# Optimization experiments

Measured on AMD Instinct MI355X. Metric: run time of the kernel, lower is better.

## Reference

```python
import jax, jax.numpy as jnp
import numpy as np
from jax import lax

B, T, F, K = 128, 1024, 128, 32


def setup_inputs() -> dict:
    key = jax.random.key(0)
    k1, k2, k3 = jax.random.split(key, 3)
    inp = jax.random.normal(k1, (B, T, F), dtype=jnp.float32)
    mask = jnp.ones((B, T), dtype=bool)
    W_emit = jax.random.normal(k2, (F, K), dtype=jnp.float32) * 0.02
    transition = jax.random.normal(k3, (K, K), dtype=jnp.float32) * 0.1
    return {"input": inp, "mask": mask, "W_emit": W_emit, "transition": transition}


def reference(input, mask, W_emit, transition):
    # emissions: [B, T, K]
    emission = jnp.einsum('btf,fk->btk', input, W_emit)
    alpha0 = emission[:, 0]                      # [B, K]
    em_seq = jnp.swapaxes(emission[:, 1:], 0, 1)  # [T-1, B, K]
    mk_seq = jnp.swapaxes(mask[:, 1:], 0, 1)      # [T-1, B]

    def step(alpha, xs):
        em_t, m_t = xs
        # alpha_t[b,j] = logsumexp_i(alpha[b,i] + transition[i,j]) + em_t[b,j]
        new = jax.scipy.special.logsumexp(alpha[:, :, None] + transition[None], axis=1) + em_t
        alpha = jnp.where(m_t[:, None], new, alpha)
        return alpha, None

    alpha, _ = lax.scan(step, alpha0, (em_seq, mk_seq))
    log_z = jax.scipy.special.logsumexp(alpha, axis=-1)  # [B]
    return jnp.sum(log_z)
```

## Files before the change

### kernel.cpp

```cpp
#include <hip/hip_runtime.h>
#include <hip/hip_bf16.h>

#define Bb 128
#define Tt 1024
#define Ff 128
#define Kk 32
#define KE 36
#define LOG32 3.4657359027997265f

typedef __attribute__((ext_vector_type(8))) short bf16x8;
typedef __attribute__((ext_vector_type(4))) float f32x4;
typedef __attribute__((ext_vector_type(16))) float f32x16;

__device__ __forceinline__ float bf2f(unsigned u) {
    return __uint_as_float(u << 16);
}
__device__ __forceinline__ unsigned bfpk2(float a, float b) {
    __hip_bfloat162 h = __float22bfloat162_rn(make_float2(a, b));
    unsigned u;
    __builtin_memcpy(&u, &h, sizeof(u));
    return u;
}
__device__ __forceinline__ void plswap(unsigned &a, unsigned &b) {
    asm("v_permlane32_swap_b32 %0, %1" : "+v"(a), "+v"(b));
}

__global__ __launch_bounds__(64, 4) void chunk_kernel(
    const float* __restrict__ inp, const int* __restrict__ mask,
    const float* __restrict__ W, const float* __restrict__ trans,
    unsigned short* __restrict__ SQ, float* __restrict__ out)
{
    __shared__ __align__(16) float gl[32 * KE];
    const int lane = threadIdx.x & 63;
    const int q = (lane >> 4) & 3, n = lane & 15;
    const int c32 = lane & 31, hi = lane >> 5;
    const int b = blockIdx.x >> 5, c = blockIdx.x & 31;
    const int t0 = c * 32;

    if (blockIdx.x == 0 && lane == 0) out[0] = 0.f;

    const int* mbp = mask + (long)b * Tt;
    unsigned mbits = (unsigned)__ballot(mbp[t0 + c32] != 0);
    if (c == 0) mbits &= ~1u;

    bf16x8 Wlo[4], Whi[4];
    #pragma unroll
    for (int kt = 0; kt < 4; ++kt) {
        const int f0 = kt * 32 + q * 8;
        float wl[8], wh[8];
        #pragma unroll
        for (int jj = 0; jj < 8; ++jj) {
            wl[jj] = W[(f0 + jj) * Kk + n];
            wh[jj] = W[(f0 + jj) * Kk + 16 + n];
        }
        uint4 uc = make_uint4(bfpk2(wl[0], wl[1]), bfpk2(wl[2], wl[3]),
                              bfpk2(wl[4], wl[5]), bfpk2(wl[6], wl[7]));
        uint4 ud = make_uint4(bfpk2(wh[0], wh[1]), bfpk2(wh[2], wh[3]),
                              bfpk2(wh[4], wh[5]), bfpk2(wh[6], wh[7]));
        Wlo[kt] = __builtin_bit_cast(bf16x8, uc);
        Whi[kt] = __builtin_bit_cast(bf16x8, ud);
    }

    const f32x4 zz = {0.f, 0.f, 0.f, 0.f};
    #pragma unroll
    for (int s = 0; s < 2; ++s) {
        f32x4 E0 = zz, E1 = zz;
        const float* xrow = inp + ((long)b * Tt + t0 + s * 16) * Ff;
        #pragma unroll
        for (int kt = 0; kt < 4; ++kt) {
            const int f0 = kt * 32 + q * 8;
            float4 a0v = *(const float4*)&xrow[n * Ff + f0];
            float4 a1v = *(const float4*)&xrow[n * Ff + f0 + 4];
            uint4 ua = make_uint4(bfpk2(a0v.x, a0v.y), bfpk2(a0v.z, a0v.w),
                                  bfpk2(a1v.x, a1v.y), bfpk2(a1v.z, a1v.w));
            bf16x8 Aw = __builtin_bit_cast(bf16x8, ua);
            E0 = __builtin_amdgcn_mfma_f32_16x16x32_bf16(Aw, Wlo[kt], E0, 0, 0, 0);
            E1 = __builtin_amdgcn_mfma_f32_16x16x32_bf16(Aw, Whi[kt], E1, 0, 0, 0);
        }
        #pragma unroll
        for (int r = 0; r < 4; ++r) {
            gl[(s * 16 + q * 4 + r) * KE + n]      = __expf(E0[r] - LOG32);
            gl[(s * 16 + q * 4 + r) * KE + 16 + n] = __expf(E1[r] - LOG32);
        }
    }

    float Elo[8], Ehi[8];
    #pragma unroll
    for (int j = 0; j < 8; ++j) {
        Elo[j] = __expf(trans[(8 * hi + j) * Kk + c32]);
        Ehi[j] = __expf(trans[(16 + 8 * hi + j) * Kk + c32]);
    }

    unsigned B1[4], B2[4];
    #pragma unroll
    for (int w2 = 0; w2 < 4; ++w2) {
        const int r0 = 8 * hi + 2 * w2;
        B1[w2] = (r0 == c32 ? 0x3f80u : 0u) | (r0 + 1 == c32 ? (0x3f80u << 16) : 0u);
        const int r2 = 16 + r0;
        B2[w2] = (r2 == c32 ? 0x3f80u : 0u) | (r2 + 1 == c32 ? (0x3f80u << 16) : 0u);
    }

    #pragma unroll
    for (int ls = 0; ls < 32; ++ls) {
        if (!((mbits >> ls) & 1u)) continue;
        const float g = gl[ls * KE + c32];
        uint4 fa = make_uint4(bfpk2(g * Elo[0], g * Elo[1]), bfpk2(g * Elo[2], g * Elo[3]),
                              bfpk2(g * Elo[4], g * Elo[5]), bfpk2(g * Elo[6], g * Elo[7]));
        uint4 fb = make_uint4(bfpk2(g * Ehi[0], g * Ehi[1]), bfpk2(g * Ehi[2], g * Ehi[3]),
                              bfpk2(g * Ehi[4], g * Ehi[5]), bfpk2(g * Ehi[6], g * Ehi[7]));
        bf16x8 Alo = __builtin_bit_cast(bf16x8, fa);
        bf16x8 Ahi = __builtin_bit_cast(bf16x8, fb);
        uint4 ub1 = make_uint4(B1[0], B1[1], B1[2], B1[3]);
        uint4 ub2 = make_uint4(B2[0], B2[1], B2[2], B2[3]);
        f32x16 Cc = {0.f, 0.f, 0.f, 0.f, 0.f, 0.f, 0.f, 0.f,
                     0.f, 0.f, 0.f, 0.f, 0.f, 0.f, 0.f, 0.f};
        Cc = __builtin_amdgcn_mfma_f32_32x32x16_bf16(Alo, __builtin_bit_cast(bf16x8, ub1), Cc, 0, 0, 0);
        Cc = __builtin_amdgcn_mfma_f32_32x32x16_bf16(Ahi, __builtin_bit_cast(bf16x8, ub2), Cc, 0, 0, 0);
        unsigned wa = bfpk2(Cc[0], Cc[1]),   wb = bfpk2(Cc[2], Cc[3]);
        unsigned xa = bfpk2(Cc[4], Cc[5]),   xb = bfpk2(Cc[6], Cc[7]);
        unsigned ya = bfpk2(Cc[8], Cc[9]),   yb = bfpk2(Cc[10], Cc[11]);
        unsigned za = bfpk2(Cc[12], Cc[13]), zb = bfpk2(Cc[14], Cc[15]);
        plswap(wa, xa); B1[0] = wa; B1[2] = xa;
        plswap(wb, xb); B1[1] = wb; B1[3] = xb;
        plswap(ya, za); B2[0] = ya; B2[2] = za;
        plswap(yb, zb); B2[1] = yb; B2[3] = zb;
    }

    unsigned short* sq = SQ + (long)(b * 32 + c) * 1024;
    #pragma unroll
    for (int w2 = 0; w2 < 4; ++w2) {
        const int r0 = 8 * hi + 2 * w2;
        sq[ r0      * 32 + c32] = (unsigned short)(B1[w2] & 0xffffu);
        sq[(r0 + 1) * 32 + c32] = (unsigned short)(B1[w2] >> 16);
        const int r2 = 16 + r0;
        sq[ r2      * 32 + c32] = (unsigned short)(B2[w2] & 0xffffu);
        sq[(r2 + 1) * 32 + c32] = (unsigned short)(B2[w2] >> 16);
    }
}

__global__ __launch_bounds__(64) void apply_kernel(
    const float* __restrict__ inp, const int* __restrict__ mask,
    const float* __restrict__ W, const unsigned short* __restrict__ SQ,
    float* __restrict__ out)
{
    const int b = blockIdx.x, lane = threadIdx.x & 63, k = lane & 31;
    const int* mbp = mask + (long)b * Tt;

    const unsigned short* sqb = SQ + (long)b * 32 * 1024;
    uint4 cur[4], nxt[4];
    #pragma unroll
    for (int e = 0; e < 4; ++e) cur[e] = *(const uint4*)(sqb + k * 32 + 8 * e);
    #pragma unroll
    for (int e = 0; e < 4; ++e) nxt[e] = *(const uint4*)(sqb + 1024 + k * 32 + 8 * e);

    int cnt = 0;
    #pragma unroll
    for (int it = 0; it < 16; ++it) cnt += (mbp[it * 64 + lane] != 0) ? 1 : 0;
    #pragma unroll
    for (int off = 32; off; off >>= 1) cnt += __shfl_xor(cnt, off);
    cnt -= (mbp[0] != 0) ? 1 : 0;

    const float* x0 = inp + (long)b * Tt * Ff;
    float a0 = 0.f;
    #pragma unroll 4
    for (int f = 0; f < Ff; ++f)
        a0 = fmaf(x0[f], W[f * Kk + k], a0);

    float c0 = __int_as_float(__builtin_amdgcn_readlane(__float_as_int(a0), 0));
    float p = __expf(a0 - c0);
    float csum = c0 + (float)cnt * LOG32;

    #pragma unroll 2
    for (int c = 0; c < 32; ++c) {
        uint4 pf[4];
        if (c + 2 < 32) {
            const unsigned short* s2 = sqb + (c + 2) * 1024 + k * 32;
            #pragma unroll
            for (int e = 0; e < 4; ++e) pf[e] = *(const uint4*)(s2 + 8 * e);
        }
        const int pi = __float_as_int(p);
        float q0 = 0.f, q1 = 0.f, q2 = 0.f, q3 = 0.f;
        #define RL(j) __int_as_float(__builtin_amdgcn_readlane(pi, (j)))
        #define ACC2(word, j, acc) \
            acc = fmaf(bf2f((word) & 0xffffu), RL(j), acc); \
            acc = fmaf(bf2f((word) >> 16),     RL((j) + 1), acc);
        ACC2(cur[0].x,  0, q0) ACC2(cur[0].y,  2, q0) ACC2(cur[0].z,  4, q0) ACC2(cur[0].w,  6, q0)
        ACC2(cur[1].x,  8, q1) ACC2(cur[1].y, 10, q1) ACC2(cur[1].z, 12, q1) ACC2(cur[1].w, 14, q1)
        ACC2(cur[2].x, 16, q2) ACC2(cur[2].y, 18, q2) ACC2(cur[2].z, 20, q2) ACC2(cur[2].w, 22, q2)
        ACC2(cur[3].x, 24, q3) ACC2(cur[3].y, 26, q3) ACC2(cur[3].z, 28, q3) ACC2(cur[3].w, 30, q3)
        #undef ACC2
        #undef RL
        float qq = (q0 + q1) + (q2 + q3);
        if (c == 15) {
            float s0 = __int_as_float(__builtin_amdgcn_readlane(__float_as_int(qq), 0));
            csum += __logf(s0);
            qq *= (1.0f / s0);
        }
        p = qq;
        #pragma unroll
        for (int e = 0; e < 4; ++e) { cur[e] = nxt[e]; nxt[e] = pf[e]; }
    }

    float sum = p;
    #pragma unroll
    for (int off = 16; off > 0; off >>= 1)
        sum += __shfl_xor(sum, off);
    if (lane == 0)
        atomicAdd(out, csum + __logf(sum));
}

extern "C" void kernel_launch(void* const* d_in, const int* in_sizes, int n_in,
                              void* d_out, int out_size, void* d_ws, size_t ws_size,
                              hipStream_t stream)
{
    const float* inp   = (const float*)d_in[0];
    const int*   mask  = (const int*)d_in[1];
    const float* W     = (const float*)d_in[2];
    const float* trans = (const float*)d_in[3];
    float* out = (float*)d_out;
    unsigned short* SQ = (unsigned short*)d_ws;

    chunk_kernel<<<dim3(Bb * 32), dim3(64), 0, stream>>>(inp, mask, W, trans, SQ, out);
    apply_kernel<<<dim3(Bb), dim3(64), 0, stream>>>(inp, mask, W, SQ, out);
}
```

Baseline: 135.5 us.

## Overlap emission loads with chain steps and store chunk products as fp32

In chunk_kernel, the input loads for both 16-step halves are issued early, and the second half's emission MFMA runs between the two halves of the chain, so global load latency is hidden behind chain work. Occupancy is lowered to make room for the extra registers. The chunk transfer matrices are now written as fp32 instead of bf16. apply_kernel keeps them in a 4-deep register ring buffer and prefetches four chunks ahead, and the initial dot product uses four independent accumulators. This doubles workspace traffic and register use in exchange for removing bf16 unpacking and exposed load latency.

```diff
diff --git a/kernel.cpp b/kernel.cpp
--- a/kernel.cpp
+++ b/kernel.cpp
@@ -25,10 +25,10 @@
     asm("v_permlane32_swap_b32 %0, %1" : "+v"(a), "+v"(b));
 }
 
-__global__ __launch_bounds__(64, 4) void chunk_kernel(
+__global__ __launch_bounds__(64, 3) void chunk_kernel(
     const float* __restrict__ inp, const int* __restrict__ mask,
     const float* __restrict__ W, const float* __restrict__ trans,
-    unsigned short* __restrict__ SQ, float* __restrict__ out)
+    float* __restrict__ SQ, float* __restrict__ out)
 {
     __shared__ __align__(16) float gl[32 * KE];
     const int lane = threadIdx.x & 63;
@@ -43,6 +43,14 @@
     unsigned mbits = (unsigned)__ballot(mbp[t0 + c32] != 0);
     if (c == 0) mbits &= ~1u;
 
+    const float* xrow = inp + ((long)b * Tt + t0) * Ff;
+    float4 x0r[8];
+    #pragma unroll
+    for (int kt = 0; kt < 4; ++kt) {
+        x0r[2 * kt]     = *(const float4*)&xrow[n * Ff + kt * 32 + q * 8];
+        x0r[2 * kt + 1] = *(const float4*)&xrow[n * Ff + kt * 32 + q * 8 + 4];
+    }
+
     bf16x8 Wlo[4], Whi[4];
     #pragma unroll
     for (int kt = 0; kt < 4; ++kt) {
@@ -62,15 +70,12 @@
     }
 
     const f32x4 zz = {0.f, 0.f, 0.f, 0.f};
-    #pragma unroll
-    for (int s = 0; s < 2; ++s) {
+
+    {
         f32x4 E0 = zz, E1 = zz;
-        const float* xrow = inp + ((long)b * Tt + t0 + s * 16) * Ff;
         #pragma unroll
         for (int kt = 0; kt < 4; ++kt) {
-            const int f0 = kt * 32 + q * 8;
-            float4 a0v = *(const float4*)&xrow[n * Ff + f0];
-            float4 a1v = *(const float4*)&xrow[n * Ff + f0 + 4];
+            float4 a0v = x0r[2 * kt], a1v = x0r[2 * kt + 1];
             uint4 ua = make_uint4(bfpk2(a0v.x, a0v.y), bfpk2(a0v.z, a0v.w),
                                   bfpk2(a1v.x, a1v.y), bfpk2(a1v.z, a1v.w));
             bf16x8 Aw = __builtin_bit_cast(bf16x8, ua);
@@ -79,9 +84,16 @@
         }
         #pragma unroll
         for (int r = 0; r < 4; ++r) {
-            gl[(s * 16 + q * 4 + r) * KE + n]      = __expf(E0[r] - LOG32);
-            gl[(s * 16 + q * 4 + r) * KE + 16 + n] = __expf(E1[r] - LOG32);
-        }
+            gl[(q * 4 + r) * KE + n]      = __expf(E0[r] - LOG32);
+            gl[(q * 4 + r) * KE + 16 + n] = __expf(E1[r] - LOG32);
+        }
+    }
+
+    float4 x1r[8];
+    #pragma unroll
+    for (int kt = 0; kt < 4; ++kt) {
+        x1r[2 * kt]     = *(const float4*)&xrow[(16 + n) * Ff + kt * 32 + q * 8];
+        x1r[2 * kt + 1] = *(const float4*)&xrow[(16 + n) * Ff + kt * 32 + q * 8 + 4];
     }
 
     float Elo[8], Ehi[8];
@@ -100,9 +112,8 @@
         B2[w2] = (r2 == c32 ? 0x3f80u : 0u) | (r2 + 1 == c32 ? (0x3f80u << 16) : 0u);
     }
 
-    #pragma unroll
-    for (int ls = 0; ls < 32; ++ls) {
-        if (!((mbits >> ls) & 1u)) continue;
+    auto chain_step = [&](int ls) {
+        if (!((mbits >> ls) & 1u)) return;
         const float g = gl[ls * KE + c32];
         uint4 fa = make_uint4(bfpk2(g * Elo[0], g * Elo[1]), bfpk2(g * Elo[2], g * Elo[3]),
                               bfpk2(g * Elo[4], g * Elo[5]), bfpk2(g * Elo[6], g * Elo[7]));
@@ -124,35 +135,61 @@
         plswap(wb, xb); B1[1] = wb; B1[3] = xb;
         plswap(ya, za); B2[0] = ya; B2[2] = za;
         plswap(yb, zb); B2[1] = yb; B2[3] = zb;
-    }
-
-    unsigned short* sq = SQ + (long)(b * 32 + c) * 1024;
+    };
+
+    #pragma unroll
+    for (int ls = 0; ls < 16; ++ls) chain_step(ls);
+
+    {
+        f32x4 E0 = zz, E1 = zz;
+        #pragma unroll
+        for (int kt = 0; kt < 4; ++kt) {
+            float4 a0v = x1r[2 * kt], a1v = x1r[2 * kt + 1];
+            uint4 ua = make_uint4(bfpk2(a0v.x, a0v.y), bfpk2(a0v.z, a0v.w),
+                                  bfpk2(a1v.x, a1v.y), bfpk2(a1v.z, a1v.w));
+            bf16x8 Aw = __builtin_bit_cast(bf16x8, ua);
+            E0 = __builtin_amdgcn_mfma_f32_16x16x32_bf16(Aw, Wlo[kt], E0, 0, 0, 0);
+            E1 = __builtin_amdgcn_mfma_f32_16x16x32_bf16(Aw, Whi[kt], E1, 0, 0, 0);
+        }
+        #pragma unroll
+        for (int r = 0; r < 4; ++r) {
+            gl[(16 + q * 4 + r) * KE + n]      = __expf(E0[r] - LOG32);
+            gl[(16 + q * 4 + r) * KE + 16 + n] = __expf(E1[r] - LOG32);
+        }
+    }
+
+    #pragma unroll
+    for (int ls = 16; ls < 32; ++ls) chain_step(ls);
+
+    float* sq = SQ + (long)(b * 32 + c) * 1024;
     #pragma unroll
     for (int w2 = 0; w2 < 4; ++w2) {
         const int r0 = 8 * hi + 2 * w2;
-        sq[ r0      * 32 + c32] = (unsigned short)(B1[w2] & 0xffffu);
-        sq[(r0 + 1) * 32 + c32] = (unsigned short)(B1[w2] >> 16);
+        sq[ r0      * 32 + c32] = bf2f(B1[w2] & 0xffffu);
+        sq[(r0 + 1) * 32 + c32] = bf2f(B1[w2] >> 16);
         const int r2 = 16 + r0;
-        sq[ r2      * 32 + c32] = (unsigned short)(B2[w2] & 0xffffu);
-        sq[(r2 + 1) * 32 + c32] = (unsigned short)(B2[w2] >> 16);
+        sq[ r2      * 32 + c32] = bf2f(B2[w2] & 0xffffu);
+        sq[(r2 + 1) * 32 + c32] = bf2f(B2[w2] >> 16);
     }
 }
 
 __global__ __launch_bounds__(64) void apply_kernel(
     const float* __restrict__ inp, const int* __restrict__ mask,
-    const float* __restrict__ W, const unsigned short* __restrict__ SQ,
+    const float* __restrict__ W, const float* __restrict__ SQ,
     float* __restrict__ out)
 {
     const int b = blockIdx.x, lane = threadIdx.x & 63, k = lane & 31;
+    const float* sqb = SQ + (long)b * 32 * 1024 + k * 32;
+
+    float Qb[4][32];
+    #pragma unroll
+    for (int pc = 0; pc < 4; ++pc) {
+        #pragma unroll
+        for (int e = 0; e < 8; ++e)
+            *(float4*)&Qb[pc][4 * e] = *(const float4*)(sqb + pc * 1024 + 4 * e);
+    }
+
     const int* mbp = mask + (long)b * Tt;
-
-    const unsigned short* sqb = SQ + (long)b * 32 * 1024;
-    uint4 cur[4], nxt[4];
-    #pragma unroll
-    for (int e = 0; e < 4; ++e) cur[e] = *(const uint4*)(sqb + k * 32 + 8 * e);
-    #pragma unroll
-    for (int e = 0; e < 4; ++e) nxt[e] = *(const uint4*)(sqb + 1024 + k * 32 + 8 * e);
-
     int cnt = 0;
     #pragma unroll
     for (int it = 0; it < 16; ++it) cnt += (mbp[it * 64 + lane] != 0) ? 1 : 0;
@@ -161,45 +198,50 @@
     cnt -= (mbp[0] != 0) ? 1 : 0;
 
     const float* x0 = inp + (long)b * Tt * Ff;
-    float a0 = 0.f;
-    #pragma unroll 4
-    for (int f = 0; f < Ff; ++f)
-        a0 = fmaf(x0[f], W[f * Kk + k], a0);
-
-    float c0 = __int_as_float(__builtin_amdgcn_readlane(__float_as_int(a0), 0));
-    float p = __expf(a0 - c0);
+    float a0 = 0.f, a1 = 0.f, a2 = 0.f, a3 = 0.f;
+    #pragma unroll 8
+    for (int f = 0; f < Ff; f += 4) {
+        a0 = fmaf(x0[f],     W[f * Kk + k],       a0);
+        a1 = fmaf(x0[f + 1], W[(f + 1) * Kk + k], a1);
+        a2 = fmaf(x0[f + 2], W[(f + 2) * Kk + k], a2);
+        a3 = fmaf(x0[f + 3], W[(f + 3) * Kk + k], a3);
+    }
+    float av = (a0 + a1) + (a2 + a3);
+
+    float c0 = __int_as_float(__builtin_amdgcn_readlane(__float_as_int(av), 0));
+    float p = __expf(av - c0);
     float csum = c0 + (float)cnt * LOG32;
 
-    #pragma unroll 2
-    for (int c = 0; c < 32; ++c) {
-        uint4 pf[4];
-        if (c + 2 < 32) {
-            const unsigned short* s2 = sqb + (c + 2) * 1024 + k * 32;
+    #define RLX(j) __int_as_float(__builtin_amdgcn_readlane(pi, (j)))
+    for (int co = 0; co < 8; ++co) {
+        #pragma unroll
+        for (int ci = 0; ci < 4; ++ci) {
+            const int cc = co * 4 + ci;
+            const int pi = __float_as_int(p);
+            float q0 = 0.f, q1 = 0.f, q2 = 0.f, q3 = 0.f;
             #pragma unroll
-            for (int e = 0; e < 4; ++e) pf[e] = *(const uint4*)(s2 + 8 * e);
-        }
-        const int pi = __float_as_int(p);
-        float q0 = 0.f, q1 = 0.f, q2 = 0.f, q3 = 0.f;
-        #define RL(j) __int_as_float(__builtin_amdgcn_readlane(pi, (j)))
-        #define ACC2(word, j, acc) \
-            acc = fmaf(bf2f((word) & 0xffffu), RL(j), acc); \
-            acc = fmaf(bf2f((word) >> 16),     RL((j) + 1), acc);
-        ACC2(cur[0].x,  0, q0) ACC2(cur[0].y,  2, q0) ACC2(cur[0].z,  4, q0) ACC2(cur[0].w,  6, q0)
-        ACC2(cur[1].x,  8, q1) ACC2(cur[1].y, 10, q1) ACC2(cur[1].z, 12, q1) ACC2(cur[1].w, 14, q1)
-        ACC2(cur[2].x, 16, q2) ACC2(cur[2].y, 18, q2) ACC2(cur[2].z, 20, q2) ACC2(cur[2].w, 22, q2)
-        ACC2(cur[3].x, 24, q3) ACC2(cur[3].y, 26, q3) ACC2(cur[3].z, 28, q3) ACC2(cur[3].w, 30, q3)
-        #undef ACC2
-        #undef RL
-        float qq = (q0 + q1) + (q2 + q3);
-        if (c == 15) {
-            float s0 = __int_as_float(__builtin_amdgcn_readlane(__float_as_int(qq), 0));
-            csum += __logf(s0);
-            qq *= (1.0f / s0);
-        }
-        p = qq;
-        #pragma unroll
-        for (int e = 0; e < 4; ++e) { cur[e] = nxt[e]; nxt[e] = pf[e]; }
-    }
+            for (int j = 0; j < 8; ++j) {
+                q0 = fmaf(Qb[ci][j],      RLX(j),      q0);
+                q1 = fmaf(Qb[ci][8 + j],  RLX(8 + j),  q1);
+                q2 = fmaf(Qb[ci][16 + j], RLX(16 + j), q2);
+                q3 = fmaf(Qb[ci][24 + j], RLX(24 + j), q3);
+            }
+            float qq = (q0 + q1) + (q2 + q3);
+            if (cc < 28) {
+                const float* s4 = sqb + (cc + 4) * 1024;
+                #pragma unroll
+                for (int e = 0; e < 8; ++e)
+                    *(float4*)&Qb[ci][4 * e] = *(const float4*)(s4 + 4 * e);
+            }
+            if (cc == 15) {
+                float s0 = __int_as_float(__builtin_amdgcn_readlane(__float_as_int(qq), 0));
+                csum += __logf(s0);
+                qq *= (1.0f / s0);
+            }
+            p = qq;
+        }
+    }
+    #undef RLX
 
     float sum = p;
     #pragma unroll
@@ -218,7 +260,7 @@
     const float* W     = (const float*)d_in[2];
     const float* trans = (const float*)d_in[3];
     float* out = (float*)d_out;
-    unsigned short* SQ = (unsigned short*)d_ws;
+    float* SQ = (float*)d_ws;
 
     chunk_kernel<<<dim3(Bb * 32), dim3(64), 0, stream>>>(inp, mask, W, trans, SQ, out);
     apply_kernel<<<dim3(Bb), dim3(64), 0, stream>>>(inp, mask, W, SQ, out);
```

New measurement: 134.0 us. About the same (-1.1%).
